# Performance work log

Measured on AMD Instinct MI355X. Metric: run time of the kernel, lower is better.

## Reference

```python
import math
import jax, jax.numpy as jnp
import numpy as np

D_MODEL = 1024
L_MAX = 4096
BATCH = 2
FILTER_ORDER = 64
EMB_DIM = 3


def _make_z(L, emb_dim=EMB_DIM):
    # PositionalEmbedding: [time, real bands, imag bands] -> [1, L, emb_dim]
    t = jnp.linspace(0.0, 1.0, L)[None, :, None]
    bands = (emb_dim - 1) // 2
    t_res = jnp.linspace(0.0, L - 1.0, L)[None, :, None]
    w = 2.0 * math.pi * t_res / L
    f = jnp.linspace(1e-4, float(bands - 1), bands)[None, None]
    ph = f * w  # z = exp(-1j*ph) -> real=cos(ph), imag=-sin(ph)
    return jnp.concatenate([t, jnp.cos(ph), -jnp.sin(ph)], axis=-1).astype(jnp.float32)


def setup_inputs() -> dict:
    key = jax.random.key(0)
    ks = jax.random.split(key, 16)
    d = D_MODEL
    iw = 3 * d  # inner_width = d_model * (order + 1), order=2

    def rn(k, shape, scale):
        return (jax.random.normal(k, shape) * scale).astype(jnp.float32)

    return {
        'u': rn(ks[0], (BATCH, L_MAX, d), 1.0),
        'w_in': rn(ks[1], (iw, d), d ** -0.5),
        'b_in': rn(ks[2], (iw,), 0.01),
        'sf_w': rn(ks[3], (iw, 1, 3), 3 ** -0.5),
        'sf_b': rn(ks[4], (iw,), 0.01),
        'z': _make_z(L_MAX),
        'w0': rn(ks[5], (FILTER_ORDER, EMB_DIM), EMB_DIM ** -0.5),
        'b0': rn(ks[6], (FILTER_ORDER,), 0.01),
        'freq': jnp.ones((1, FILTER_ORDER), dtype=jnp.float32),  # Sin(w=1)
        'w1': rn(ks[7], (FILTER_ORDER, FILTER_ORDER), FILTER_ORDER ** -0.5),
        'b1': rn(ks[8], (FILTER_ORDER,), 0.01),
        'w2': rn(ks[9], (FILTER_ORDER, FILTER_ORDER), FILTER_ORDER ** -0.5),
        'b2': rn(ks[10], (FILTER_ORDER,), 0.01),
        'wf': rn(ks[11], (d, FILTER_ORDER), FILTER_ORDER ** -0.5),
        'D': rn(ks[12], (d,), 1.0),
        'w_out': rn(ks[13], (d, d), d ** -0.5),
        'b_out': rn(ks[14], (d,), 0.01),
    }


def _dwconv(x, w, b):
    # depthwise Conv1d(kernel=3, padding=2, groups=C); x: [B, C, L] -> [B, C, L+2]
    y = jax.lax.conv_general_dilated(
        x, w, window_strides=(1,), padding=[(2, 2)],
        feature_group_count=x.shape[1],
        dimension_numbers=('NCH', 'OIH', 'NCH'))
    return y + b[None, :, None]


def _fftconv(v, k, D):
    # circular conv via zero-padded FFT; torch's k_f/fft_size with norm='forward'
    # irfft cancels to the standard (norm='backward') inverse.
    L = v.shape[-1]
    n = 2 * L
    y = jnp.fft.irfft(jnp.fft.rfft(v, n=n) * jnp.fft.rfft(k, n=n), n=n)[..., :L]
    return y + v * D[:, None]


def reference(u, w_in, b_in, sf_w, sf_b, z, w0, b0, freq, w1, b1, w2, b2, wf, D, w_out, b_out):
    b, l, d = u.shape
    L = min(l, L_MAX)

    # input projection + short depthwise filter
    up = jnp.einsum('bld,ed->ble', u, w_in) + b_in  # [b, l, 3d]
    up = up.transpose(0, 2, 1)                       # [b, 3d, l]
    uc = _dwconv(up, sf_w, sf_b)[..., :L]            # [b, 3d, L]
    x0, x1, v = jnp.split(uc, 3, axis=1)             # each [b, d, L]

    # implicit filter MLP with shared Sin activation
    h = jnp.sin(freq * (z @ w0.T + b0))              # [1, L, 64]
    h = jnp.sin(freq * (h @ w1.T + b1))
    h = jnp.sin(freq * (h @ w2.T + b2))
    h = h @ wf.T                                     # [1, L, d]

    # exponential modulation (buffers: t, deltas)
    t = jnp.linspace(0.0, 1.0, L)[None, :, None]
    max_decay = math.log(0.01) / 0.3
    min_decay = math.log(0.01) / 1.5
    deltas = jnp.linspace(min_decay, max_decay, d)[None, None]
    h = h * jnp.exp(-t * jnp.abs(deltas))            # [1, L, d]
    k = h[0].T                                       # [d, L]

    # hyena recurrence (order=2 -> one gated fft conv)
    v = _fftconv(v * x1, k, D)
    y = (v * x0).transpose(0, 2, 1)                  # [b, L, d]
    return jnp.einsum('bld,ed->ble', y, w_out) + b_out
```

## Files before the change

### kernel.cpp

```cpp
#include <hip/hip_runtime.h>
#include <math.h>

#define DM   1024
#define LL   4096
#define NB   2
#define E3   3072
#define FPI  3.14159265358979323846f

typedef __bf16 bf16x8 __attribute__((ext_vector_type(8)));
typedef float  f32x4  __attribute__((ext_vector_type(4)));
typedef _Float16 f16x2 __attribute__((ext_vector_type(2)));

__device__ __forceinline__ unsigned short f2bf(float x) {
    unsigned u = __float_as_uint(x);
    u += 0x7fffu + ((u >> 16) & 1u);
    return (unsigned short)(u >> 16);
}
__device__ __forceinline__ float bf2f(ushort s) {
    return __uint_as_float(((unsigned)s) << 16);
}
__device__ __forceinline__ void gload16(void* lds, const void* g) {
    typedef const __attribute__((address_space(1))) unsigned int* gp_t;
    typedef __attribute__((address_space(3))) unsigned int* lp_t;
    __builtin_amdgcn_global_load_lds((gp_t)g, (lp_t)lds, 16, 0, 0);
}

__global__ __launch_bounds__(256) void k_cvt3(
    const float* __restrict__ a, ushort* __restrict__ oa, int n4a,
    const float* __restrict__ b, ushort* __restrict__ ob, int n4b,
    const float* __restrict__ c, ushort* __restrict__ oc, int n4c)
{
    int idx = blockIdx.x * 256 + threadIdx.x;
    int stride = gridDim.x * 256;
    int tot = n4a + n4b + n4c;
    for (int i = idx; i < tot; i += stride) {
        const float4* src; ushort* dst; int k;
        if (i < n4a)            { src = (const float4*)a; dst = oa; k = i; }
        else if (i < n4a + n4b) { src = (const float4*)b; dst = ob; k = i - n4a; }
        else                    { src = (const float4*)c; dst = oc; k = i - n4a - n4b; }
        float4 v = src[k];
        ushort4 o;
        o.x = f2bf(v.x); o.y = f2bf(v.y); o.z = f2bf(v.z); o.w = f2bf(v.w);
        *reinterpret_cast<ushort4*>(dst + 4 * k) = o;
    }
}

__global__ __launch_bounds__(512, 1) void k_gemm128n(
    const ushort* __restrict__ A, const ushort* __restrict__ B,
    const float* __restrict__ bias, ushort* __restrict__ C,
    int Ntiles, int ldc)
{
    __shared__ __align__(16) char ldsm[98304];
    const int tid  = threadIdx.x;
    const int lane = tid & 63;
    const int w    = tid >> 6;
    const int wr   = w >> 2, wc = w & 3;

    const int cpx = gridDim.x >> 3;
    int swz = (blockIdx.x & 7) * cpx + (blockIdx.x >> 3);
    const int m0 = (swz / Ntiles) << 7;
    const int n0 = (swz % Ntiles) << 8;

    const int r0 = tid >> 2;
    const int swzc = ((tid & 3) ^ ((r0 >> 1) & 3)) << 4;
    const char* Asrc = (const char*)A + ((size_t)(m0 + r0) << 11) + swzc;
    const char* Bsrc = (const char*)B + ((size_t)(n0 + r0) << 11) + swzc;
    char* Ld = ldsm + tid * 16;

    const int lm = lane & 15, lk = lane >> 4;
    const int rA = wr * 64 + lm;
    const int rB = wc * 64 + lm;
    const int aBase = rA * 64 + ((lk ^ ((rA >> 1) & 3)) << 4);
    const int bBase = 16384 + rB * 64 + ((lk ^ ((rB >> 1) & 3)) << 4);

#define STG_A(ks, nb, t1) \
    gload16(Ld + (nb) + (ks)*8192, Asrc + (t1)*128 + (ks)*64)
#define STG_B(ks, nb, t1) do { \
    gload16(Ld + (nb) + 16384 + (ks)*16384,        Bsrc + (t1)*128 + (ks)*64); \
    gload16(Ld + (nb) + 16384 + (ks)*16384 + 8192, Bsrc + (t1)*128 + (ks)*64 + 262144); } while(0)
#define LDA(buf, ks, m) (*(const bf16x8*)(ldsm + (buf) + (ks)*8192 + aBase + (m)*1024))
#define LDB(buf, ks, n) (*(const bf16x8*)(ldsm + (buf) + (ks)*16384 + bBase + (n)*1024))
#define VMCNT3() asm volatile("s_waitcnt vmcnt(3)" ::: "memory")
#define VMCNT0() asm volatile("s_waitcnt vmcnt(0)" ::: "memory")
#define BAR() __builtin_amdgcn_s_barrier()

    f32x4 acc[4][4];
#pragma unroll
    for (int i = 0; i < 4; ++i)
#pragma unroll
        for (int j = 0; j < 4; ++j)
#pragma unroll
            for (int r = 0; r < 4; ++r) acc[i][j][r] = 0.f;

    STG_A(0, 0, 0); STG_B(0, 0, 0); STG_A(1, 0, 0); STG_B(1, 0, 0);
    VMCNT3();
    BAR();

    bf16x8 af[2], bq[4];
#pragma unroll 1
    for (int t = 0; t < 15; ++t) {
        const int buf = (t & 1) * 49152;
        const int nb  = 49152 - buf;
        const int t1  = t + 1;
#pragma unroll
        for (int n = 0; n < 4; ++n) bq[n] = LDB(buf, 0, n);
        af[0] = LDA(buf, 0, 0); af[1] = LDA(buf, 0, 1);
        STG_A(0, nb, t1);
        BAR();
        __builtin_amdgcn_s_setprio(1);
#pragma unroll
        for (int m = 0; m < 2; ++m)
#pragma unroll
            for (int n = 0; n < 4; ++n)
                acc[m][n] = __builtin_amdgcn_mfma_f32_16x16x32_bf16(af[m], bq[n], acc[m][n], 0, 0, 0);
        __builtin_amdgcn_s_setprio(0);
        BAR();
        af[0] = LDA(buf, 0, 2); af[1] = LDA(buf, 0, 3);
        STG_B(0, nb, t1);
        VMCNT3();
        BAR();
        __builtin_amdgcn_s_setprio(1);
#pragma unroll
        for (int m = 0; m < 2; ++m)
#pragma unroll
            for (int n = 0; n < 4; ++n)
                acc[2 + m][n] = __builtin_amdgcn_mfma_f32_16x16x32_bf16(af[m], bq[n], acc[2 + m][n], 0, 0, 0);
        __builtin_amdgcn_s_setprio(0);
        BAR();
#pragma unroll
        for (int n = 0; n < 4; ++n) bq[n] = LDB(buf, 1, n);
        af[0] = LDA(buf, 1, 0); af[1] = LDA(buf, 1, 1);
        STG_A(1, nb, t1);
        BAR();
        __builtin_amdgcn_s_setprio(1);
#pragma unroll
        for (int m = 0; m < 2; ++m)
#pragma unroll
            for (int n = 0; n < 4; ++n)
                acc[m][n] = __builtin_amdgcn_mfma_f32_16x16x32_bf16(af[m], bq[n], acc[m][n], 0, 0, 0);
        __builtin_amdgcn_s_setprio(0);
        BAR();
        af[0] = LDA(buf, 1, 2); af[1] = LDA(buf, 1, 3);
        STG_B(1, nb, t1);
        VMCNT3();
        BAR();
        __builtin_amdgcn_s_setprio(1);
#pragma unroll
        for (int m = 0; m < 2; ++m)
#pragma unroll
            for (int n = 0; n < 4; ++n)
                acc[2 + m][n] = __builtin_amdgcn_mfma_f32_16x16x32_bf16(af[m], bq[n], acc[2 + m][n], 0, 0, 0);
        __builtin_amdgcn_s_setprio(0);
        BAR();
    }
    {
        const int buf = 49152;
#pragma unroll
        for (int n = 0; n < 4; ++n) bq[n] = LDB(buf, 0, n);
        af[0] = LDA(buf, 0, 0); af[1] = LDA(buf, 0, 1);
#pragma unroll
        for (int m = 0; m < 2; ++m)
#pragma unroll
            for (int n = 0; n < 4; ++n)
                acc[m][n] = __builtin_amdgcn_mfma_f32_16x16x32_bf16(af[m], bq[n], acc[m][n], 0, 0, 0);
        af[0] = LDA(buf, 0, 2); af[1] = LDA(buf, 0, 3);
#pragma unroll
        for (int m = 0; m < 2; ++m)
#pragma unroll
            for (int n = 0; n < 4; ++n)
                acc[2 + m][n] = __builtin_amdgcn_mfma_f32_16x16x32_bf16(af[m], bq[n], acc[2 + m][n], 0, 0, 0);
        VMCNT0();
        BAR();
#pragma unroll
        for (int n = 0; n < 4; ++n) bq[n] = LDB(buf, 1, n);
        af[0] = LDA(buf, 1, 0); af[1] = LDA(buf, 1, 1);
#pragma unroll
        for (int m = 0; m < 2; ++m)
#pragma unroll
            for (int n = 0; n < 4; ++n)
                acc[m][n] = __builtin_amdgcn_mfma_f32_16x16x32_bf16(af[m], bq[n], acc[m][n], 0, 0, 0);
        af[0] = LDA(buf, 1, 2); af[1] = LDA(buf, 1, 3);
#pragma unroll
        for (int m = 0; m < 2; ++m)
#pragma unroll
            for (int n = 0; n < 4; ++n)
                acc[2 + m][n] = __builtin_amdgcn_mfma_f32_16x16x32_bf16(af[m], bq[n], acc[2 + m][n], 0, 0, 0);
    }
    const int er = lk << 2, ec = lm;
#pragma unroll
    for (int m = 0; m < 4; ++m) {
        int row = m0 + wr * 64 + m * 16 + er;
#pragma unroll
        for (int n = 0; n < 4; ++n) {
            int col = n0 + wc * 64 + n * 16 + ec;
            float bz = bias[col];
            ushort* cp = C + (size_t)row * ldc + col;
#pragma unroll
            for (int r = 0; r < 4; ++r)
                cp[(size_t)r * ldc] = f2bf(acc[m][n][r] + bz);
        }
    }
#undef STG_A
#undef STG_B
#undef LDA
#undef LDB
#undef VMCNT3
#undef VMCNT0
#undef BAR
}

__global__ __launch_bounds__(256) void k_gemm_bf16(
    const ushort* __restrict__ A, const ushort* __restrict__ B,
    const float* __restrict__ bias, float* __restrict__ C, int ldc)
{
    __shared__ ushort As[128 * 32];
    __shared__ ushort Bs[128 * 32];
    const int tid  = threadIdx.x;
    const int lane = tid & 63;
    const int w    = tid >> 6;
    const int wm   = (w >> 1) << 6, wn = (w & 1) << 6;
    const int m0   = blockIdx.y << 7, n0 = blockIdx.x << 7;

    f32x4 acc[4][4];
#pragma unroll
    for (int i = 0; i < 4; ++i)
#pragma unroll
        for (int j = 0; j < 4; ++j)
#pragma unroll
            for (int r = 0; r < 4; ++r) acc[i][j][r] = 0.f;

    const char* Ab = (const char*)A + ((size_t)(m0 + (tid >> 2)) << 11) + ((tid & 3) << 4);
    const char* Bb = (const char*)B + ((size_t)(n0 + (tid >> 2)) << 11) + ((tid & 3) << 4);
    char* AsD = (char*)As + tid * 16;
    char* BsD = (char*)Bs + tid * 16;
    const char* ap = (const char*)As + ((wm + (lane & 15)) << 6) + ((lane >> 4) << 4);
    const char* bp = (const char*)Bs + ((wn + (lane & 15)) << 6) + ((lane >> 4) << 4);

    for (int k0 = 0; k0 < 1024; k0 += 32) {
        __syncthreads();
        gload16(AsD,        Ab + k0 * 2);
        gload16(AsD + 4096, Ab + 131072 + k0 * 2);
        gload16(BsD,        Bb + k0 * 2);
        gload16(BsD + 4096, Bb + 131072 + k0 * 2);
        __syncthreads();
        bf16x8 af[4], bfr[4];
#pragma unroll
        for (int i = 0; i < 4; ++i) {
            af[i]  = *(const bf16x8*)(ap + (i << 10));
            bfr[i] = *(const bf16x8*)(bp + (i << 10));
        }
#pragma unroll
        for (int i = 0; i < 4; ++i)
#pragma unroll
            for (int j = 0; j < 4; ++j)
                acc[i][j] = __builtin_amdgcn_mfma_f32_16x16x32_bf16(
                    af[i], bfr[j], acc[i][j], 0, 0, 0);
    }
    const int er = (lane >> 4) << 2;
    const int ec = lane & 15;
#pragma unroll
    for (int i = 0; i < 4; ++i) {
        int row = m0 + wm + (i << 4) + er;
#pragma unroll
        for (int j = 0; j < 4; ++j) {
            int col = n0 + wn + (j << 4) + ec;
            float bz = bias[col];
            float* cp = C + (size_t)row * ldc + col;
#pragma unroll
            for (int r = 0; r < 4; ++r)
                cp[(size_t)r * ldc] = acc[i][j][r] + bz;
        }
    }
}

__global__ __launch_bounds__(256) void k_dwconv(
    const ushort* __restrict__ up, const float* __restrict__ sfw,
    const float* __restrict__ sfb, ushort* __restrict__ x0t,
    float* __restrict__ vin)
{
    __shared__ float xT[32][65];
    __shared__ float vT[32][65];
    const int b  = blockIdx.z;
    const int t0 = blockIdx.y * 64;
    const int c0 = blockIdx.x * 32;
    const int tid = threadIdx.x;
    const int cL = tid & 31, tL = tid >> 5;
    const ushort* upb = up + (size_t)b * LL * E3;
    const int c = c0 + cL;

#pragma unroll
    for (int r = 0; r < 8; ++r) {
        int t_local = (r << 3) + tL;
        int t = t0 + t_local;
        float res[3];
#pragma unroll
        for (int s3 = 0; s3 < 3; ++s3) {
            int e = c + (s3 << 10);
            float w0 = sfw[e*3+0], w1 = sfw[e*3+1], w2 = sfw[e*3+2];
            float xa = (t >= 2) ? bf2f(upb[(size_t)(t-2)*E3 + e]) : 0.f;
            float xb = (t >= 1) ? bf2f(upb[(size_t)(t-1)*E3 + e]) : 0.f;
            float xc = bf2f(upb[(size_t)t*E3 + e]);
            res[s3] = w0*xa + w1*xb + w2*xc + sfb[e];
        }
        xT[cL][t_local] = res[0];
        vT[cL][t_local] = res[1] * res[2];
    }
    __syncthreads();
    const int cW = tid >> 3, q = tid & 7;
    size_t off = ((size_t)b * DM + c0 + cW) * LL + t0 + 8*q;
    ushort xb16[8] __attribute__((aligned(16)));
#pragma unroll
    for (int i = 0; i < 8; ++i) xb16[i] = f2bf(xT[cW][8*q + i]);
    *reinterpret_cast<uint4*>(x0t + off) = *reinterpret_cast<uint4*>(xb16);
    float tmp[8];
#pragma unroll
    for (int i = 0; i < 8; ++i) tmp[i] = vT[cW][8*q + i];
    *reinterpret_cast<float4*>(vin + off)     = make_float4(tmp[0], tmp[1], tmp[2], tmp[3]);
    *reinterpret_cast<float4*>(vin + off + 4) = make_float4(tmp[4], tmp[5], tmp[6], tmp[7]);
}

__global__ __launch_bounds__(256) void k_filt_mlp(
    const float* __restrict__ z, const float* __restrict__ w0,
    const float* __restrict__ b0, const float* __restrict__ fr,
    const float* __restrict__ w1, const float* __restrict__ b1,
    const float* __restrict__ w2, const float* __restrict__ b2,
    float* __restrict__ H3)
{
    __shared__ float w1t[64 * 65];
    __shared__ float w2t[64 * 65];
    __shared__ float hb[4][64];
    const int tid = threadIdx.x;
    for (int idx = tid; idx < 4096; idx += 256) {
        int j = idx >> 6, m = idx & 63;
        w1t[m*65 + j] = w1[idx];
        w2t[m*65 + j] = w2[idx];
    }
    __syncthreads();
    const int tl = tid >> 6, j = tid & 63;
    const float frj = fr[j];
    const float b0j = b0[j], b1j = b1[j], b2j = b2[j];
    const float w00 = w0[j*3+0], w01 = w0[j*3+1], w02 = w0[j*3+2];
    const int t0 = blockIdx.x * 16;
    for (int r = 0; r < 4; ++r) {
        int t = t0 + r*4 + tl;
        float z0 = z[t*3+0], z1 = z[t*3+1], z2 = z[t*3+2];
        float h = sinf(frj * (b0j + z0*w00 + z1*w01 + z2*w02));
        hb[tl][j] = h;
        __syncthreads();
        float s = b1j;
#pragma unroll
        for (int m = 0; m < 64; ++m) s = fmaf(hb[tl][m], w1t[m*65 + j], s);
        __syncthreads();
        h = sinf(frj * s);
        hb[tl][j] = h;
        __syncthreads();
        s = b2j;
#pragma unroll
        for (int m = 0; m < 64; ++m) s = fmaf(hb[tl][m], w2t[m*65 + j], s);
        h = sinf(frj * s);
        H3[(size_t)t * 64 + j] = h;
        __syncthreads();
    }
}

__global__ __launch_bounds__(256) void k_filt_k(
    const float* __restrict__ H3, const float* __restrict__ wf,
    float* __restrict__ kf)
{
    __shared__ float Hs[64][65];
    __shared__ float Ws[64][65];
    const int tid = threadIdx.x;
    const int t0 = blockIdx.x * 64, d0 = blockIdx.y * 64;
    for (int idx = tid; idx < 4096; idx += 256) {
        int r = idx >> 6, cc = idx & 63;
        Hs[r][cc] = H3[(size_t)(t0 + r) * 64 + cc];
        Ws[r][cc] = wf[(size_t)(d0 + r) * 64 + cc];
    }
    __syncthreads();
    const int tx = tid & 15, ty = tid >> 4;
    float acc[4][4];
#pragma unroll
    for (int i = 0; i < 4; ++i)
#pragma unroll
        for (int jj = 0; jj < 4; ++jj) acc[i][jj] = 0.f;
#pragma unroll
    for (int j = 0; j < 64; ++j) {
        float wv[4], hv[4];
#pragma unroll
        for (int i = 0; i < 4; ++i) wv[i] = Ws[4*ty + i][j];
#pragma unroll
        for (int i = 0; i < 4; ++i) hv[i] = Hs[4*tx + i][j];
#pragma unroll
        for (int i = 0; i < 4; ++i)
#pragma unroll
            for (int jj = 0; jj < 4; ++jj) acc[i][jj] = fmaf(wv[i], hv[jj], acc[i][jj]);
    }
    const float mind = -3.0701134573253944f;
    const float maxd = -15.350567286626972f;
#pragma unroll
    for (int i = 0; i < 4; ++i) {
        int d = d0 + 4*ty + i;
        float delta = fabsf(mind + (maxd - mind) * ((float)d / 1023.f));
#pragma unroll
        for (int jj = 0; jj < 4; ++jj) {
            int t = t0 + 4*tx + jj;
            float tn = (float)t / 4095.f;
            kf[(size_t)d * LL + t] = acc[i][jj] * expf(-tn * delta);
        }
    }
}

__device__ __forceinline__ int pidx(int p) { return p + (p >> 4); }

__device__ __forceinline__ float2 cmul(float2 a, float2 b) {
    return make_float2(a.x*b.x - a.y*b.y, a.x*b.y + a.y*b.x);
}

__device__ void fft_lds_fwd4(float2* buf, int tid) {
    int lh = 10;
#pragma unroll
    for (int h = 2048; h >= 32; h >>= 2, lh -= 2) {
        const int hh = h >> 1;
        const float rinv = -FPI / (float)h;
        __syncthreads();
#pragma unroll
        for (int r = 0; r < 4; ++r) {
            int bf = (r << 9) + tid;
            int q  = bf & (hh - 1);
            int g  = bf >> lh;
            int j  = (g << (lh + 2)) + q;
            float2 a = buf[pidx(j)];
            float2 b = buf[pidx(j + hh)];
            float2 c = buf[pidx(j + h)];
            float2 d = buf[pidx(j + h + hh)];
            float2 t0 = make_float2(a.x + c.x, a.y + c.y);
            float2 t1 = make_float2(a.x - c.x, a.y - c.y);
            float2 t2 = make_float2(b.x + d.x, b.y + d.y);
            float2 t3 = make_float2(b.y - d.y, d.x - b.x);
            float sn, cs;
            __sincosf(rinv * (float)q, &sn, &cs);
            float c2 = cs*cs - sn*sn, s2 = 2.f*cs*sn;
            float c3 = cs*c2 - sn*s2, s3 = cs*s2 + sn*c2;
            buf[pidx(j)] = make_float2(t0.x + t2.x, t0.y + t2.y);
            float2 e1 = make_float2(t0.x - t2.x, t0.y - t2.y);
            buf[pidx(j + hh)] = make_float2(e1.x*c2 - e1.y*s2, e1.x*s2 + e1.y*c2);
            float2 e2 = make_float2(t1.x + t3.x, t1.y + t3.y);
            buf[pidx(j + h)] = make_float2(e2.x*cs - e2.y*sn, e2.x*sn + e2.y*cs);
            float2 e3 = make_float2(t1.x - t3.x, t1.y - t3.y);
            buf[pidx(j + h + hh)] = make_float2(e3.x*c3 - e3.y*s3, e3.x*s3 + e3.y*c3);
        }
    }
    __syncthreads();
}

__device__ void fft_lds_inv4(float2* buf, int tid) {
    int lh = 4;
#pragma unroll
    for (int h = 32; h <= 2048; h <<= 2, lh += 2) {
        const int hh = h >> 1;
        const float rpos = FPI / (float)h;
        __syncthreads();
#pragma unroll
        for (int r = 0; r < 4; ++r) {
            int bf = (r << 9) + tid;
            int q  = bf & (hh - 1);
            int g  = bf >> lh;
            int j  = (g << (lh + 2)) + q;
            float2 o0 = buf[pidx(j)];
            float2 o1 = buf[pidx(j + hh)];
            float2 o2 = buf[pidx(j + h)];
            float2 o3 = buf[pidx(j + h + hh)];
            float sn, cs;
            __sincosf(rpos * (float)q, &sn, &cs);
            float c2 = cs*cs - sn*sn, s2 = 2.f*cs*sn;
            float c3 = cs*c2 - sn*s2, s3 = cs*s2 + sn*c2;
            float2 p1 = make_float2(o1.x*c2 - o1.y*s2, o1.x*s2 + o1.y*c2);
            float2 p2 = make_float2(o2.x*cs - o2.y*sn, o2.x*sn + o2.y*cs);
            float2 p3 = make_float2(o3.x*c3 - o3.y*s3, o3.x*s3 + o3.y*c3);
            float2 u0 = make_float2(o0.x + p1.x, o0.y + p1.y);
            float2 u1 = make_float2(o0.x - p1.x, o0.y - p1.y);
            float2 u2 = make_float2(p2.x + p3.x, p2.y + p3.y);
            float2 u3 = make_float2(p2.x - p3.x, p2.y - p3.y);
            float2 ib = make_float2(-u3.y, u3.x);
            buf[pidx(j)]          = make_float2(u0.x + u2.x, u0.y + u2.y);
            buf[pidx(j + hh)]     = make_float2(u1.x + ib.x, u1.y + ib.y);
            buf[pidx(j + h)]      = make_float2(u0.x - u2.x, u0.y - u2.y);
            buf[pidx(j + h + hh)] = make_float2(u1.x - ib.x, u1.y - ib.y);
        }
    }
    __syncthreads();
}

__device__ __forceinline__ void fft_reg_fwd(float2* c) {
    const float W16r[8] = {1.f, 0.92387953f, 0.70710678f, 0.38268343f,
                           0.f, -0.38268343f, -0.70710678f, -0.92387953f};
    const float W16i[8] = {0.f, -0.38268343f, -0.70710678f, -0.92387953f,
                           -1.f, -0.92387953f, -0.70710678f, -0.38268343f};
#pragma unroll
    for (int k = 0; k < 8; ++k) {
        float2 a = c[k], b = c[k+8];
        float2 d = make_float2(a.x - b.x, a.y - b.y);
        c[k]   = make_float2(a.x + b.x, a.y + b.y);
        c[k+8] = cmul(d, make_float2(W16r[k], W16i[k]));
    }
    const float W8r[4] = {1.f, 0.70710678f, 0.f, -0.70710678f};
    const float W8i[4] = {0.f, -0.70710678f, -1.f, -0.70710678f};
#pragma unroll
    for (int blk = 0; blk < 16; blk += 8)
#pragma unroll
        for (int k = 0; k < 4; ++k) {
            float2 a = c[blk+k], b = c[blk+k+4];
            float2 d = make_float2(a.x - b.x, a.y - b.y);
            c[blk+k]   = make_float2(a.x + b.x, a.y + b.y);
            c[blk+k+4] = cmul(d, make_float2(W8r[k], W8i[k]));
        }
#pragma unroll
    for (int blk = 0; blk < 16; blk += 4) {
        {   float2 a = c[blk], b = c[blk+2];
            c[blk]   = make_float2(a.x + b.x, a.y + b.y);
            c[blk+2] = make_float2(a.x - b.x, a.y - b.y); }
        {   float2 a = c[blk+1], b = c[blk+3];
            float2 d = make_float2(a.x - b.x, a.y - b.y);
            c[blk+1] = make_float2(a.x + b.x, a.y + b.y);
            c[blk+3] = make_float2(d.y, -d.x); }
    }
#pragma unroll
    for (int blk = 0; blk < 16; blk += 2) {
        float2 a = c[blk], b = c[blk+1];
        c[blk]   = make_float2(a.x + b.x, a.y + b.y);
        c[blk+1] = make_float2(a.x - b.x, a.y - b.y);
    }
}

__device__ __forceinline__ void fft_reg_inv(float2* c) {
#pragma unroll
    for (int blk = 0; blk < 16; blk += 2) {
        float2 a = c[blk], b = c[blk+1];
        c[blk]   = make_float2(a.x + b.x, a.y + b.y);
        c[blk+1] = make_float2(a.x - b.x, a.y - b.y);
    }
#pragma unroll
    for (int blk = 0; blk < 16; blk += 4) {
        {   float2 a = c[blk], b = c[blk+2];
            c[blk]   = make_float2(a.x + b.x, a.y + b.y);
            c[blk+2] = make_float2(a.x - b.x, a.y - b.y); }
        {   float2 a = c[blk+1], b = c[blk+3];
            float2 bt = make_float2(-c[blk+3].y, c[blk+3].x);
            c[blk+1] = make_float2(a.x + bt.x, a.y + bt.y);
            c[blk+3] = make_float2(a.x - bt.x, a.y - bt.y); }
    }
    const float W8r[4] = {1.f, 0.70710678f, 0.f, -0.70710678f};
    const float W8i[4] = {0.f, 0.70710678f, 1.f, 0.70710678f};
#pragma unroll
    for (int blk = 0; blk < 16; blk += 8)
#pragma unroll
        for (int k = 0; k < 4; ++k) {
            float2 a = c[blk+k], b = c[blk+k+4];
            float2 bt = cmul(b, make_float2(W8r[k], W8i[k]));
            c[blk+k]   = make_float2(a.x + bt.x, a.y + bt.y);
            c[blk+k+4] = make_float2(a.x - bt.x, a.y - bt.y);
        }
    const float W16r[8] = {1.f, 0.92387953f, 0.70710678f, 0.38268343f,
                           0.f, -0.38268343f, -0.70710678f, -0.92387953f};
    const float W16i[8] = {0.f, 0.38268343f, 0.70710678f, 0.92387953f,
                           1.f, 0.92387953f, 0.70710678f, 0.38268343f};
#pragma unroll
    for (int k = 0; k < 8; ++k) {
        float2 a = c[k], b = c[k+8];
        float2 bt = cmul(b, make_float2(W16r[k], W16i[k]));
        c[k]   = make_float2(a.x + bt.x, a.y + bt.y);
        c[k+8] = make_float2(a.x - bt.x, a.y - bt.y);
    }
}

__global__ __launch_bounds__(512) void k_kfft(
    const float* __restrict__ kf, f16x2* __restrict__ Kf)
{
    __shared__ float2 buf[8704];
    const int d = blockIdx.x, tid = threadIdx.x;
    const float* krow = kf + (size_t)d * LL;
    const float rinv0 = -FPI / 4096.f;
    for (int i = tid; i < 1024; i += 512) {
        float4 k4 = reinterpret_cast<const float4*>(krow)[i];
        int p = 4 * i;
        float kv[4] = {k4.x, k4.y, k4.z, k4.w};
#pragma unroll
        for (int q = 0; q < 4; ++q) {
            float sn, cs;
            __sincosf(rinv0 * (float)(p + q), &sn, &cs);
            buf[pidx(p + q)]        = make_float2(kv[q], 0.f);
            buf[pidx(p + q + 4096)] = make_float2(kv[q] * cs, kv[q] * sn);
        }
    }
    fft_lds_fwd4(buf, tid);
    float2 c[16];
    const int p0 = tid * 16;
#pragma unroll
    for (int j = 0; j < 16; ++j) c[j] = buf[pidx(p0 + j)];
    fft_reg_fwd(c);
    f16x2* outp = Kf + (size_t)d * 8192 + p0;
#pragma unroll
    for (int j = 0; j < 16; ++j) {
        f16x2 o;
        o[0] = (_Float16)(c[j].x * (1.f/8192.f));
        o[1] = (_Float16)(c[j].y * (1.f/8192.f));
        outp[j] = o;
    }
}

__global__ __launch_bounds__(512) void k_fftconv(
    const float* __restrict__ vin, const f16x2* __restrict__ Kf,
    const ushort* __restrict__ x0t, const float* __restrict__ Dp,
    ushort* __restrict__ yg)
{
    __shared__ float2 buf[8704];
    const int d = blockIdx.x, tid = threadIdx.x;
    const float* vrow0 = vin + (size_t)d * LL;
    const float* vrow1 = vin + ((size_t)DM + d) * LL;
    const float rinv0 = -FPI / 4096.f;
    float vs0[8], vs1[8];
#pragma unroll
    for (int ii = 0; ii < 2; ++ii) {
        int i = tid + ii * 512;
        float4 a4 = reinterpret_cast<const float4*>(vrow0)[i];
        float4 b4 = reinterpret_cast<const float4*>(vrow1)[i];
        int p = 4 * i;
        float ar[4] = {a4.x, a4.y, a4.z, a4.w};
        float br[4] = {b4.x, b4.y, b4.z, b4.w};
#pragma unroll
        for (int q = 0; q < 4; ++q) {
            vs0[ii*4 + q] = ar[q];
            vs1[ii*4 + q] = br[q];
            float sn, cs;
            __sincosf(rinv0 * (float)(p + q), &sn, &cs);
            float2 z = make_float2(ar[q], br[q]);
            buf[pidx(p + q)]        = z;
            buf[pidx(p + q + 4096)] = cmul(z, make_float2(cs, sn));
        }
    }
    fft_lds_fwd4(buf, tid);
    float2 c[16];
    const int p0 = tid * 16;
#pragma unroll
    for (int j = 0; j < 16; ++j) c[j] = buf[pidx(p0 + j)];
    fft_reg_fwd(c);
    const f16x2* kfr = Kf + (size_t)d * 8192 + p0;
#pragma unroll
    for (int j = 0; j < 16; ++j) {
        f16x2 kv = kfr[j];
        c[j] = cmul(c[j], make_float2((float)kv[0], (float)kv[1]));
    }
    fft_reg_inv(c);
#pragma unroll
    for (int j = 0; j < 16; ++j) buf[pidx(p0 + j)] = c[j];
    fft_lds_inv4(buf, tid);
    const float Dd = Dp[d];
    const ushort* xrow0 = x0t + (size_t)d * LL;
    const ushort* xrow1 = x0t + ((size_t)DM + d) * LL;
    ushort* orow0 = yg + (size_t)d * LL;
    ushort* orow1 = yg + ((size_t)DM + d) * LL;
    const float rinv4 = FPI / 4096.f;
#pragma unroll
    for (int ii = 0; ii < 2; ++ii) {
        int i = tid + ii * 512;
        ushort4 x40 = reinterpret_cast<const ushort4*>(xrow0)[i];
        ushort4 x41 = reinterpret_cast<const ushort4*>(xrow1)[i];
        float xr0[4] = {bf2f(x40.x), bf2f(x40.y), bf2f(x40.z), bf2f(x40.w)};
        float xr1[4] = {bf2f(x41.x), bf2f(x41.y), bf2f(x41.z), bf2f(x41.w)};
        int p = 4 * i;
        ushort s0[4], s1[4];
#pragma unroll
        for (int q = 0; q < 4; ++q) {
            float sn, cs;
            __sincosf(rinv4 * (float)(p + q), &sn, &cs);
            float2 a  = buf[pidx(p + q)];
            float2 bb = buf[pidx(p + q + 4096)];
            float2 bt = cmul(bb, make_float2(cs, sn));
            float yre = a.x + bt.x;
            float yim = a.y + bt.y;
            s0[q] = f2bf((yre + Dd * vs0[ii*4 + q]) * xr0[q]);
            s1[q] = f2bf((yim + Dd * vs1[ii*4 + q]) * xr1[q]);
        }
        *reinterpret_cast<ushort4*>(orow0 + p) = make_ushort4(s0[0], s0[1], s0[2], s0[3]);
        *reinterpret_cast<ushort4*>(orow1 + p) = make_ushort4(s1[0], s1[1], s1[2], s1[3]);
    }
}

__global__ __launch_bounds__(256) void k_tr(
    const ushort* __restrict__ yg, ushort* __restrict__ Ag)
{
    __shared__ ushort S[64][72];
    const int b  = blockIdx.z;
    const int d0 = blockIdx.y * 64;
    const int t0 = blockIdx.x * 64;
    const int tid = threadIdx.x;
#pragma unroll
    for (int p = 0; p < 2; ++p) {
        int idx = p * 256 + tid;
        int dr = idx >> 3, c8 = (idx & 7) << 3;
        uint4 v = *reinterpret_cast<const uint4*>(
            yg + ((size_t)b * DM + d0 + dr) * LL + t0 + c8);
        *reinterpret_cast<uint4*>(&S[dr][c8]) = v;
    }
    __syncthreads();
#pragma unroll
    for (int p = 0; p < 2; ++p) {
        int idx = p * 256 + tid;
        int tr = idx >> 3, dq = (idx & 7) << 3;
        ushort tmp[8] __attribute__((aligned(16)));
#pragma unroll
        for (int q = 0; q < 8; ++q) tmp[q] = S[dq + q][tr];
        *reinterpret_cast<uint4*>(Ag + ((size_t)b * LL + t0 + tr) * DM + d0 + dq) =
            *reinterpret_cast<uint4*>(tmp);
    }
}

extern "C" void kernel_launch(void* const* d_in, const int* in_sizes, int n_in,
                              void* d_out, int out_size, void* d_ws, size_t ws_size,
                              hipStream_t stream)
{
    if (n_in < 17) return;
    const float* u    = (const float*)d_in[0];
    const float* w_in = (const float*)d_in[1];
    const float* b_in = (const float*)d_in[2];
    const float* sf_w = (const float*)d_in[3];
    const float* sf_b = (const float*)d_in[4];
    const float* z    = (const float*)d_in[5];
    const float* w0   = (const float*)d_in[6];
    const float* b0   = (const float*)d_in[7];
    const float* freq = (const float*)d_in[8];
    const float* w1   = (const float*)d_in[9];
    const float* b1   = (const float*)d_in[10];
    const float* w2   = (const float*)d_in[11];
    const float* b2   = (const float*)d_in[12];
    const float* wf   = (const float*)d_in[13];
    const float* Dp   = (const float*)d_in[14];
    const float* wout = (const float*)d_in[15];
    const float* bout = (const float*)d_in[16];
    float* out = (float*)d_out;
    float* ws  = (float*)d_ws;

    ushort* up    = (ushort*)ws;
    f16x2*  Kf    = (f16x2*)ws;
    float*  kfbuf = ws + 16777216;
    ushort* yg    = (ushort*)(ws + 16777216);
    float*  H3    = ws + 20971520;
    ushort* Ag    = (ushort*)(ws + 20971520);
    ushort* ub    = (ushort*)(ws + 25165824);
    ushort* x0t   = (ushort*)(ws + 25165824);
    ushort* wb    = (ushort*)(ws + 33554432);
    float*  vin   = ws + 33554432;
    ushort* woutb = (ushort*)(ws + 41943040);
    const size_t NEED = (size_t)42205184 * 4;
    if (ws_size < NEED) return;

    hipLaunchKernelGGL(k_cvt3,     dim3(2048), dim3(256), 0, stream,
                       u, ub, 2097152, w_in, wb, 786432, wout, woutb, 262144);
    hipLaunchKernelGGL(k_gemm128n, dim3((8192/128) * (E3/256)), dim3(512), 0, stream,
                       ub, wb, b_in, up, E3/256, E3);
    hipLaunchKernelGGL(k_dwconv,   dim3(DM/32, LL/64, NB), dim3(256), 0, stream,
                       up, sf_w, sf_b, x0t, vin);
    hipLaunchKernelGGL(k_filt_mlp, dim3(LL/16), dim3(256), 0, stream,
                       z, w0, b0, freq, w1, b1, w2, b2, H3);
    hipLaunchKernelGGL(k_filt_k,   dim3(LL/64, DM/64), dim3(256), 0, stream,
                       H3, wf, kfbuf);
    hipLaunchKernelGGL(k_kfft,     dim3(DM), dim3(512), 0, stream,
                       kfbuf, Kf);
    hipLaunchKernelGGL(k_fftconv,  dim3(DM), dim3(512), 0, stream,
                       vin, Kf, x0t, Dp, yg);
    hipLaunchKernelGGL(k_tr,       dim3(LL/64, DM/64, NB), dim3(256), 0, stream,
                       yg, Ag);
    hipLaunchKernelGGL(k_gemm_bf16, dim3(DM/128, 8192/128), dim3(256), 0, stream,
                       Ag, woutb, bout, out, DM);
}
```

Baseline: 273.4 us.

## Compute input projection transposed and fuse depthwise conv into FFT conv kernel

The input projection GEMM now swaps operands so it writes the projection channel-major ([3d, b*L]), with bias indexed by row. That lets the separate depthwise-conv kernel and its intermediate x0t/vin buffers be removed. The FFT conv kernel reads the three bf16 channel rows directly and applies the 3-tap conv and gating inline. This removes one kernel launch and a full write and read of the fp32/bf16 intermediates, at the cost of slightly redundant halo loads and more work per block inside the FFT kernel.

```diff
diff --git a/kernel.cpp b/kernel.cpp
--- a/kernel.cpp
+++ b/kernel.cpp
@@ -193,11 +193,10 @@
 #pragma unroll
         for (int n = 0; n < 4; ++n) {
             int col = n0 + wc * 64 + n * 16 + ec;
-            float bz = bias[col];
             ushort* cp = C + (size_t)row * ldc + col;
 #pragma unroll
             for (int r = 0; r < 4; ++r)
-                cp[(size_t)r * ldc] = f2bf(acc[m][n][r] + bz);
+                cp[(size_t)r * ldc] = f2bf(acc[m][n][r] + bias[row + r]);
         }
     }
 #undef STG_A
@@ -271,52 +270,6 @@
                 cp[(size_t)r * ldc] = acc[i][j][r] + bz;
         }
     }
-}
-
-__global__ __launch_bounds__(256) void k_dwconv(
-    const ushort* __restrict__ up, const float* __restrict__ sfw,
-    const float* __restrict__ sfb, ushort* __restrict__ x0t,
-    float* __restrict__ vin)
-{
-    __shared__ float xT[32][65];
-    __shared__ float vT[32][65];
-    const int b  = blockIdx.z;
-    const int t0 = blockIdx.y * 64;
-    const int c0 = blockIdx.x * 32;
-    const int tid = threadIdx.x;
-    const int cL = tid & 31, tL = tid >> 5;
-    const ushort* upb = up + (size_t)b * LL * E3;
-    const int c = c0 + cL;
-
-#pragma unroll
-    for (int r = 0; r < 8; ++r) {
-        int t_local = (r << 3) + tL;
-        int t = t0 + t_local;
-        float res[3];
-#pragma unroll
-        for (int s3 = 0; s3 < 3; ++s3) {
-            int e = c + (s3 << 10);
-            float w0 = sfw[e*3+0], w1 = sfw[e*3+1], w2 = sfw[e*3+2];
-            float xa = (t >= 2) ? bf2f(upb[(size_t)(t-2)*E3 + e]) : 0.f;
-            float xb = (t >= 1) ? bf2f(upb[(size_t)(t-1)*E3 + e]) : 0.f;
-            float xc = bf2f(upb[(size_t)t*E3 + e]);
-            res[s3] = w0*xa + w1*xb + w2*xc + sfb[e];
-        }
-        xT[cL][t_local] = res[0];
-        vT[cL][t_local] = res[1] * res[2];
-    }
-    __syncthreads();
-    const int cW = tid >> 3, q = tid & 7;
-    size_t off = ((size_t)b * DM + c0 + cW) * LL + t0 + 8*q;
-    ushort xb16[8] __attribute__((aligned(16)));
-#pragma unroll
-    for (int i = 0; i < 8; ++i) xb16[i] = f2bf(xT[cW][8*q + i]);
-    *reinterpret_cast<uint4*>(x0t + off) = *reinterpret_cast<uint4*>(xb16);
-    float tmp[8];
-#pragma unroll
-    for (int i = 0; i < 8; ++i) tmp[i] = vT[cW][8*q + i];
-    *reinterpret_cast<float4*>(vin + off)     = make_float4(tmp[0], tmp[1], tmp[2], tmp[3]);
-    *reinterpret_cast<float4*>(vin + off + 4) = make_float4(tmp[4], tmp[5], tmp[6], tmp[7]);
 }
 
 __global__ __launch_bounds__(256) void k_filt_mlp(
@@ -608,32 +561,64 @@
     }
 }
 
+__device__ __forceinline__ void conv4(const ushort* __restrict__ row, int p,
+    float w0, float w1, float w2, float bias, float* out)
+{
+    float xm2, xm1;
+    if (p >= 2) {
+        unsigned prev = *reinterpret_cast<const unsigned*>(row + p - 2);
+        xm2 = bf2f((ushort)(prev & 0xffffu));
+        xm1 = bf2f((ushort)(prev >> 16));
+    } else { xm2 = 0.f; xm1 = 0.f; }
+    uint2 cur = *reinterpret_cast<const uint2*>(row + p);
+    float x0 = bf2f((ushort)(cur.x & 0xffffu));
+    float x1 = bf2f((ushort)(cur.x >> 16));
+    float x2 = bf2f((ushort)(cur.y & 0xffffu));
+    float x3 = bf2f((ushort)(cur.y >> 16));
+    out[0] = fmaf(w2, x0, fmaf(w1, xm1, fmaf(w0, xm2, bias)));
+    out[1] = fmaf(w2, x1, fmaf(w1, x0,  fmaf(w0, xm1, bias)));
+    out[2] = fmaf(w2, x2, fmaf(w1, x1,  fmaf(w0, x0,  bias)));
+    out[3] = fmaf(w2, x3, fmaf(w1, x2,  fmaf(w0, x1,  bias)));
+}
+
 __global__ __launch_bounds__(512) void k_fftconv(
-    const float* __restrict__ vin, const f16x2* __restrict__ Kf,
-    const ushort* __restrict__ x0t, const float* __restrict__ Dp,
-    ushort* __restrict__ yg)
+    const ushort* __restrict__ up2, const f16x2* __restrict__ Kf,
+    const float* __restrict__ sfw, const float* __restrict__ sfb,
+    const float* __restrict__ Dp, ushort* __restrict__ yg)
 {
     __shared__ float2 buf[8704];
     const int d = blockIdx.x, tid = threadIdx.x;
-    const float* vrow0 = vin + (size_t)d * LL;
-    const float* vrow1 = vin + ((size_t)DM + d) * LL;
+    const ushort* vrow0  = up2 + (size_t)(2048 + d) * 8192;
+    const ushort* vrow1  = vrow0 + 4096;
+    const ushort* x1row0 = up2 + (size_t)(1024 + d) * 8192;
+    const ushort* x1row1 = x1row0 + 4096;
+    const ushort* x0row0 = up2 + (size_t)d * 8192;
+    const ushort* x0row1 = x0row0 + 4096;
+    const float wv0 = sfw[(2048+d)*3+0], wv1 = sfw[(2048+d)*3+1],
+                wv2 = sfw[(2048+d)*3+2], bv = sfb[2048+d];
+    const float wx0 = sfw[(1024+d)*3+0], wx1 = sfw[(1024+d)*3+1],
+                wx2 = sfw[(1024+d)*3+2], bx = sfb[1024+d];
+    const float g0 = sfw[d*3+0], g1 = sfw[d*3+1], g2 = sfw[d*3+2], bg = sfb[d];
     const float rinv0 = -FPI / 4096.f;
+
     float vs0[8], vs1[8];
 #pragma unroll
     for (int ii = 0; ii < 2; ++ii) {
-        int i = tid + ii * 512;
-        float4 a4 = reinterpret_cast<const float4*>(vrow0)[i];
-        float4 b4 = reinterpret_cast<const float4*>(vrow1)[i];
-        int p = 4 * i;
-        float ar[4] = {a4.x, a4.y, a4.z, a4.w};
-        float br[4] = {b4.x, b4.y, b4.z, b4.w};
+        int p = 4 * tid + ii * 2048;
+        float cv0[4], cv1[4], cx0[4], cx1[4];
+        conv4(vrow0,  p, wv0, wv1, wv2, bv, cv0);
+        conv4(vrow1,  p, wv0, wv1, wv2, bv, cv1);
+        conv4(x1row0, p, wx0, wx1, wx2, bx, cx0);
+        conv4(x1row1, p, wx0, wx1, wx2, bx, cx1);
 #pragma unroll
         for (int q = 0; q < 4; ++q) {
-            vs0[ii*4 + q] = ar[q];
-            vs1[ii*4 + q] = br[q];
+            float z0 = cv0[q] * cx0[q];
+            float z1 = cv1[q] * cx1[q];
+            vs0[ii*4 + q] = z0;
+            vs1[ii*4 + q] = z1;
             float sn, cs;
             __sincosf(rinv0 * (float)(p + q), &sn, &cs);
-            float2 z = make_float2(ar[q], br[q]);
+            float2 z = make_float2(z0, z1);
             buf[pidx(p + q)]        = z;
             buf[pidx(p + q + 4096)] = cmul(z, make_float2(cs, sn));
         }
@@ -655,19 +640,15 @@
     for (int j = 0; j < 16; ++j) buf[pidx(p0 + j)] = c[j];
     fft_lds_inv4(buf, tid);
     const float Dd = Dp[d];
-    const ushort* xrow0 = x0t + (size_t)d * LL;
-    const ushort* xrow1 = x0t + ((size_t)DM + d) * LL;
     ushort* orow0 = yg + (size_t)d * LL;
     ushort* orow1 = yg + ((size_t)DM + d) * LL;
     const float rinv4 = FPI / 4096.f;
 #pragma unroll
     for (int ii = 0; ii < 2; ++ii) {
-        int i = tid + ii * 512;
-        ushort4 x40 = reinterpret_cast<const ushort4*>(xrow0)[i];
-        ushort4 x41 = reinterpret_cast<const ushort4*>(xrow1)[i];
-        float xr0[4] = {bf2f(x40.x), bf2f(x40.y), bf2f(x40.z), bf2f(x40.w)};
-        float xr1[4] = {bf2f(x41.x), bf2f(x41.y), bf2f(x41.z), bf2f(x41.w)};
-        int p = 4 * i;
+        int p = 4 * tid + ii * 2048;
+        float cg0[4], cg1[4];
+        conv4(x0row0, p, g0, g1, g2, bg, cg0);
+        conv4(x0row1, p, g0, g1, g2, bg, cg1);
         ushort s0[4], s1[4];
 #pragma unroll
         for (int q = 0; q < 4; ++q) {
@@ -676,10 +657,8 @@
             float2 a  = buf[pidx(p + q)];
             float2 bb = buf[pidx(p + q + 4096)];
             float2 bt = cmul(bb, make_float2(cs, sn));
-            float yre = a.x + bt.x;
-            float yim = a.y + bt.y;
-            s0[q] = f2bf((yre + Dd * vs0[ii*4 + q]) * xr0[q]);
-            s1[q] = f2bf((yim + Dd * vs1[ii*4 + q]) * xr1[q]);
+            s0[q] = f2bf((a.x + bt.x + Dd * vs0[ii*4 + q]) * cg0[q]);
+            s1[q] = f2bf((a.y + bt.y + Dd * vs1[ii*4 + q]) * cg1[q]);
         }
         *reinterpret_cast<ushort4*>(orow0 + p) = make_ushort4(s0[0], s0[1], s0[2], s0[3]);
         *reinterpret_cast<ushort4*>(orow1 + p) = make_ushort4(s1[0], s1[1], s1[2], s1[3]);
@@ -740,26 +719,22 @@
     float* out = (float*)d_out;
     float* ws  = (float*)d_ws;
 
-    ushort* up    = (ushort*)ws;
-    f16x2*  Kf    = (f16x2*)ws;
+    ushort* up2   = (ushort*)ws;
     float*  kfbuf = ws + 16777216;
     ushort* yg    = (ushort*)(ws + 16777216);
     float*  H3    = ws + 20971520;
     ushort* Ag    = (ushort*)(ws + 20971520);
     ushort* ub    = (ushort*)(ws + 25165824);
-    ushort* x0t   = (ushort*)(ws + 25165824);
     ushort* wb    = (ushort*)(ws + 33554432);
-    float*  vin   = ws + 33554432;
+    f16x2*  Kf    = (f16x2*)(ws + 33554432);
     ushort* woutb = (ushort*)(ws + 41943040);
-    const size_t NEED = (size_t)42205184 * 4;
+    const size_t NEED = (size_t)(41943040 + 524288) * 4;
     if (ws_size < NEED) return;
 
     hipLaunchKernelGGL(k_cvt3,     dim3(2048), dim3(256), 0, stream,
                        u, ub, 2097152, w_in, wb, 786432, wout, woutb, 262144);
-    hipLaunchKernelGGL(k_gemm128n, dim3((8192/128) * (E3/256)), dim3(512), 0, stream,
-                       ub, wb, b_in, up, E3/256, E3);
-    hipLaunchKernelGGL(k_dwconv,   dim3(DM/32, LL/64, NB), dim3(256), 0, stream,
-                       up, sf_w, sf_b, x0t, vin);
+    hipLaunchKernelGGL(k_gemm128n, dim3((E3/128) * (8192/256)), dim3(512), 0, stream,
+                       wb, ub, b_in, up2, 8192/256, 8192);
     hipLaunchKernelGGL(k_filt_mlp, dim3(LL/16), dim3(256), 0, stream,
                        z, w0, b0, freq, w1, b1, w2, b2, H3);
     hipLaunchKernelGGL(k_filt_k,   dim3(LL/64, DM/64), dim3(256), 0, stream,
@@ -767,7 +742,7 @@
     hipLaunchKernelGGL(k_kfft,     dim3(DM), dim3(512), 0, stream,
                        kfbuf, Kf);
     hipLaunchKernelGGL(k_fftconv,  dim3(DM), dim3(512), 0, stream,
-                       vin, Kf, x0t, Dp, yg);
+                       up2, Kf, sf_w, sf_b, Dp, yg);
     hipLaunchKernelGGL(k_tr,       dim3(LL/64, DM/64, NB), dim3(256), 0, stream,
                        yg, Ag);
     hipLaunchKernelGGL(k_gemm_bf16, dim3(DM/128, 8192/128), dim3(256), 0, stream,
```

New measurement: 223.8 us. 18.2% less time.
